# Kernel tuning notes

Measured on AMD Instinct MI355X. Metric: run time of the kernel, lower is better.

## Reference

```python
import jax, jax.numpy as jnp
import numpy as np
import math

N = 100000      # nodes per type
E = 1000000     # edges per edge type
C = 64          # hid_dim_conv (= in_channels)
H = 4           # heads
D = C // H      # head dim
L = 4           # num_conv_layers
T = 3           # node types: op, port, const
REL = [(0, 0), (0, 1), (1, 0), (1, 2), (2, 0)]  # (src_type, dst_type) per edge type
R = len(REL)
POOL = 8
PDIM = 32       # pooling_dim = max(C//2, out_channels)


def _gelu(x):
    return jax.nn.gelu(x, approximate=False)  # torch F.gelu default (erf)


def _seg_softmax(a, seg, n):
    m = jax.ops.segment_max(a, seg, num_segments=n)
    m = jnp.where(jnp.isfinite(m), m, 0.0)
    e = jnp.exp(a - m[seg])
    s = jax.ops.segment_sum(e, seg, num_segments=n)
    return e / (s[seg] + 1e-16)


def _layernorm(x, w, b):
    mu = x.mean(-1, keepdims=True)
    var = ((x - mu) ** 2).mean(-1, keepdims=True)
    return (x - mu) / jnp.sqrt(var + 1e-5) * w + b


def _forward(floats, ints):
    (x0, x1, x2, Wk, bk, Wq, bq, Wv, bv, Wa, ba, skip, ln_w, ln_b,
     a_rel, m_rel, p_rel, Wfc, bfc, Wsc, W1, b1, W2, b2, W3, b3, W4, b4) = floats
    eis = ints
    xs = [x0, x1, x2]
    inv_sqrt_d = 1.0 / math.sqrt(D)
    for l in range(L):
        k = [(xs[t] @ Wk[l, t] + bk[l, t]).reshape(N, H, D) for t in range(T)]
        q = [(xs[t] @ Wq[l, t] + bq[l, t]).reshape(N, H, D) for t in range(T)]
        v = [(xs[t] @ Wv[l, t] + bv[l, t]).reshape(N, H, D) for t in range(T)]
        out = [jnp.zeros((N, H, D), xs[0].dtype) for _ in range(T)]
        for r, (s, d) in enumerate(REL):
            ke = jnp.einsum('nhd,hde->nhe', k[s], a_rel[l, r])  # per-relation key transform
            ve = jnp.einsum('nhd,hde->nhe', v[s], m_rel[l, r])  # per-relation message transform
            row, col = eis[r][0], eis[r][1]
            al = (q[d][col] * ke[row]).sum(-1) * p_rel[l, r] * inv_sqrt_d  # [E,H]
            al = _seg_softmax(al, col, N)
            out[d] = out[d] + jax.ops.segment_sum(ve[row] * al[:, :, None], col, num_segments=N)
        nxs = []
        for t in range(T):
            o = _gelu(out[t].reshape(N, H * D)) @ Wa[l, t] + ba[l, t]
            a = jax.nn.sigmoid(skip[l, t])
            o = a * o + (1.0 - a) * xs[t]
            o = _layernorm(o, ln_w[l, t], ln_b[l, t])
            nxs.append(_gelu(o))
        xs = nxs
    # per-type node_fc, then SAG-style global top-k pooling
    zs = [_gelu(xs[t] @ Wfc[t] + bfc[t]) for t in range(T)]
    z = jnp.concatenate(zs, 0)                              # [T*N, PDIM]
    sc = jnp.concatenate([zs[t] @ Wsc[t] for t in range(T)], 0)  # [T*N]
    ts, ti = jax.lax.top_k(sc, POOL)
    pooled = z[ti] * jnp.tanh(ts)[:, None]                  # [POOL, PDIM]
    h = pooled.reshape(1, POOL * PDIM)
    h = _gelu(h @ W1 + b1)
    h = _gelu(h @ W2 + b2)
    h = _gelu(h @ W3 + b3)
    return jnp.nan_to_num(h @ W4 + b4)


def setup_inputs() -> dict:
    key = jax.random.key(0)
    ks = jax.random.split(key, 24)
    f = jnp.float32
    d = {}
    d['x_op'] = jax.random.normal(ks[0], (N, C), f)
    d['x_port'] = jax.random.normal(ks[1], (N, C), f)
    d['x_const'] = jax.random.normal(ks[2], (N, C), f)
    for i in range(R):
        d[f'ei_{i}'] = jax.random.randint(ks[3 + i], (2, E), 0, N, dtype=jnp.int32)
    s_c = 1.0 / math.sqrt(C)
    s_d = 1.0 / math.sqrt(D)
    d['Wk'] = jax.random.normal(ks[8], (L, T, C, C), f) * s_c
    d['bk'] = jnp.zeros((L, T, C), f)
    d['Wq'] = jax.random.normal(ks[9], (L, T, C, C), f) * s_c
    d['bq'] = jnp.zeros((L, T, C), f)
    d['Wv'] = jax.random.normal(ks[10], (L, T, C, C), f) * s_c
    d['bv'] = jnp.zeros((L, T, C), f)
    d['Wa'] = jax.random.normal(ks[11], (L, T, C, C), f) * s_c
    d['ba'] = jnp.zeros((L, T, C), f)
    d['skip'] = jnp.ones((L, T), f)
    d['ln_w'] = jnp.full((L, T, C), math.sqrt(2.0 / C), f)
    d['ln_b'] = jax.random.normal(ks[12], (L, T, C), f) * 0.01
    d['a_rel'] = jax.random.normal(ks[13], (L, R, H, D, D), f) * s_d
    d['m_rel'] = jax.random.normal(ks[14], (L, R, H, D, D), f) * s_d
    d['p_rel'] = jnp.ones((L, R, H), f)
    d['Wfc'] = jax.random.normal(ks[15], (T, C, PDIM), f) * s_c
    d['bfc'] = jnp.zeros((T, PDIM), f)
    d['Wsc'] = jax.random.normal(ks[16], (T, PDIM), f) * (1.0 / math.sqrt(PDIM))
    d['W1'] = jax.random.normal(ks[17], (POOL * PDIM, 128), f) * (1.0 / math.sqrt(POOL * PDIM))
    d['b1'] = jnp.zeros((128,), f)
    d['W2'] = jax.random.normal(ks[18], (128, 64), f) * (1.0 / math.sqrt(128))
    d['b2'] = jnp.zeros((64,), f)
    d['W3'] = jax.random.normal(ks[19], (64, 32), f) * (1.0 / math.sqrt(64))
    d['b3'] = jnp.zeros((32,), f)
    d['W4'] = jax.random.normal(ks[20], (32, 1), f) * (1.0 / math.sqrt(32))
    d['b4'] = jnp.zeros((1,), f)
    return d


def reference(x_op, x_port, x_const, ei_0, ei_1, ei_2, ei_3, ei_4,
              Wk, bk, Wq, bq, Wv, bv, Wa, ba, skip, ln_w, ln_b,
              a_rel, m_rel, p_rel, Wfc, bfc, Wsc,
              W1, b1, W2, b2, W3, b3, W4, b4):
    floats = (x_op, x_port, x_const, Wk, bk, Wq, bq, Wv, bv, Wa, ba, skip, ln_w, ln_b,
              a_rel, m_rel, p_rel, Wfc, bfc, Wsc, W1, b1, W2, b2, W3, b3, W4, b4)
    ints = (ei_0, ei_1, ei_2, ei_3, ei_4)
    return _forward(floats, ints)
```

## Files before the change

kernel.cpp:

```cpp
#include <hip/hip_runtime.h>
#include <math.h>
#include <float.h>

#define NN 100000
#define EE 1000000
#define CC 64
#define HH 4
#define DD 16
#define LL 4
#define TT 3
#define RR 5
#define NB 196
#define PR 64

__device__ __constant__ int g_dst[RR]   = {0, 1, 0, 2, 0};
__device__ __constant__ int g_first[RR] = {1, 1, 0, 1, 0};

__device__ __forceinline__ float geluf(float x) {
    return 0.5f * x * (1.0f + erff(x * 0.7071067811865476f));
}

__global__ void zero_out_kernel(float* out) {
    if (threadIdx.x == 0 && blockIdx.x == 0) out[0] = 0.f;
}

__device__ __forceinline__ const int* sel_edge(int r, const int* p0, const int* p1,
                                               const int* p2, const int* p3, const int* p4) {
    return (r == 0) ? p0 : (r == 1) ? p1 : (r == 2) ? p2 : (r == 3) ? p3 : p4;
}

__global__ __launch_bounds__(256) void fuse_q(
    const float* __restrict__ Wq, const float* __restrict__ bq,
    const float* __restrict__ a_rel,
    float* __restrict__ WQE, float* __restrict__ BQE)
{
    int lr = blockIdx.x;
    int l = lr / RR, r = lr % RR;
    int d = g_dst[r];
    const float* W  = Wq + (size_t)(l * TT + d) * CC * CC;
    const float* bb = bq + (size_t)(l * TT + d) * CC;
    const float* A  = a_rel + (size_t)lr * HH * DD * DD;
    float* Wo = WQE + (size_t)lr * CC * CC;
    float* bo = BQE + (size_t)lr * CC;

    for (int i = threadIdx.x; i < CC * CC; i += 256) {
        int c = i >> 6, j = i & 63, h = j >> 4, dout = j & 15;
        float acc = 0.f;
        #pragma unroll
        for (int e0 = 0; e0 < DD; ++e0)
            acc += W[c * CC + h * DD + e0] * A[(h * DD + dout) * DD + e0];
        Wo[i] = acc;
    }
    if (threadIdx.x < CC) {
        int j = threadIdx.x, h = j >> 4, dout = j & 15;
        float acc = 0.f;
        #pragma unroll
        for (int e0 = 0; e0 < DD; ++e0)
            acc += bb[h * DD + e0] * A[(h * DD + dout) * DD + e0];
        bo[j] = acc;
    }
}

__global__ __launch_bounds__(256) void bucket_hist(
    const int* __restrict__ p0, const int* __restrict__ p1, const int* __restrict__ p2,
    const int* __restrict__ p3, const int* __restrict__ p4, int* __restrict__ bcnt)
{
    int r = blockIdx.y;
    const int* col = sel_edge(r, p0, p1, p2, p3, p4) + EE;
    __shared__ int lh[256];
    int tid = threadIdx.x;
    lh[tid] = 0;
    __syncthreads();
    int base = blockIdx.x * 4096;
    for (int i = tid; i < 4096; i += 256) {
        int g = base + i;
        if (g < EE) atomicAdd(&lh[col[g] >> 9], 1);
    }
    __syncthreads();
    if (tid < NB && lh[tid]) atomicAdd(&bcnt[r * NB + tid], lh[tid]);
}

__global__ __launch_bounds__(256) void bucket_scan(
    const int* __restrict__ bcnt, int* __restrict__ bbase, int* __restrict__ gcur,
    int* __restrict__ indptr)
{
    int r = blockIdx.x;
    __shared__ int ls[256];
    int tid = threadIdx.x;
    ls[tid] = (tid < NB) ? bcnt[r * NB + tid] : 0;
    __syncthreads();
    for (int o = 1; o < 256; o <<= 1) {
        int v = (tid >= o) ? ls[tid - o] : 0;
        __syncthreads();
        ls[tid] += v;
        __syncthreads();
    }
    int ex = (tid == 0) ? 0 : ls[tid - 1];
    if (tid < NB) {
        bbase[r * (NB + 1) + tid] = ex;
        gcur[r * NB + tid] = ex;
    }
    if (tid == NB) bbase[r * (NB + 1) + NB] = ls[NB - 1];
    if (tid == 0) indptr[(size_t)r * (NN + 1) + NN] = EE;
}

__global__ __launch_bounds__(256) void bucket_partition(
    const int* __restrict__ p0, const int* __restrict__ p1, const int* __restrict__ p2,
    const int* __restrict__ p3, const int* __restrict__ p4,
    int* __restrict__ gcur, unsigned* __restrict__ pairs)
{
    int r = blockIdx.y;
    const int* ebase = sel_edge(r, p0, p1, p2, p3, p4);
    const int* colp = ebase + EE;
    __shared__ int2 stag[4096];
    __shared__ int lh[256], lofs[256], lcur[256], gpos[256];
    int tid = threadIdx.x;
    lh[tid] = 0;
    __syncthreads();
    int base = blockIdx.x * 4096;
    for (int i = tid; i < 4096; i += 256) {
        int g = base + i;
        if (g < EE) atomicAdd(&lh[colp[g] >> 9], 1);
    }
    __syncthreads();
    lofs[tid] = lh[tid];
    __syncthreads();
    for (int o = 1; o < 256; o <<= 1) {
        int v = (tid >= o) ? lofs[tid - o] : 0;
        __syncthreads();
        lofs[tid] += v;
        __syncthreads();
    }
    int ex = (tid == 0) ? 0 : lofs[tid - 1];
    __syncthreads();
    lofs[tid] = ex;
    lcur[tid] = ex;
    gpos[tid] = (lh[tid] > 0) ? atomicAdd(&gcur[r * NB + tid], lh[tid]) : 0;
    __syncthreads();
    for (int i = tid; i < 4096; i += 256) {
        int g = base + i;
        if (g < EE) {
            int c = colp[g];
            int b = c >> 9;
            int s = atomicAdd(&lcur[b], 1);
            stag[s] = make_int2(ebase[g], c);
        }
    }
    __syncthreads();
    int total = EE - base; if (total > 4096) total = 4096;
    for (int s = tid; s < total; s += 256) {
        int2 pr = stag[s];
        int b = pr.y >> 9;
        unsigned packed = ((unsigned)(pr.y & 511) << 17) | (unsigned)pr.x;
        pairs[(size_t)r * EE + gpos[b] + (s - lofs[b])] = packed;
    }
}

__global__ __launch_bounds__(256) void bucket_finalize(
    const unsigned* __restrict__ pairs, const int* __restrict__ bbase,
    int* __restrict__ indptr, int* __restrict__ rowsrt)
{
    int r = blockIdx.y, b = blockIdx.x;
    int beg = bbase[r * (NB + 1) + b], end = bbase[r * (NB + 1) + b + 1];
    int d0 = b << 9;
    int nd = NN - d0; if (nd > 512) nd = 512;
    __shared__ int cnt[512];
    __shared__ int exc[512];
    __shared__ int ls[256];
    int tid = threadIdx.x;
    cnt[tid] = 0; cnt[tid + 256] = 0;
    __syncthreads();
    const unsigned* pp = pairs + (size_t)r * EE;
    for (int e = beg + tid; e < end; e += 256)
        atomicAdd(&cnt[pp[e] >> 17], 1);
    __syncthreads();
    int a0 = cnt[2 * tid], a1 = cnt[2 * tid + 1];
    ls[tid] = a0 + a1;
    __syncthreads();
    for (int o = 1; o < 256; o <<= 1) {
        int v = (tid >= o) ? ls[tid - o] : 0;
        __syncthreads();
        ls[tid] += v;
        __syncthreads();
    }
    int ex2 = (tid == 0) ? 0 : ls[tid - 1];
    exc[2 * tid] = ex2;
    exc[2 * tid + 1] = ex2 + a0;
    __syncthreads();
    for (int i = tid; i < nd; i += 256)
        indptr[(size_t)r * (NN + 1) + d0 + i] = beg + exc[i];
    cnt[2 * tid] = exc[2 * tid];
    cnt[2 * tid + 1] = exc[2 * tid + 1];
    __syncthreads();
    for (int e = beg + tid; e < end; e += 256) {
        unsigned pr = pp[e];
        int p = atomicAdd(&cnt[pr >> 17], 1);
        rowsrt[(size_t)r * EE + beg + p] = (int)(pr & 0x1FFFFu);
    }
}

__global__ __launch_bounds__(256) void projKV_kernel(
    const float* __restrict__ X,
    const float* __restrict__ WK, const float* __restrict__ BK,
    const float* __restrict__ WV, const float* __restrict__ BV,
    float* __restrict__ KV, int nrows)
{
    __shared__ float Xs[PR][CC + 1];
    __shared__ float WKs[CC][CC];
    __shared__ float WVs[CC][CC];
    __shared__ float bks[CC], bvs[CC];
    int tid = threadIdx.x;
    int row0 = blockIdx.x * PR;
    for (int i = tid; i < CC * CC; i += 256) {
        WKs[i >> 6][i & 63] = WK[i];
        WVs[i >> 6][i & 63] = WV[i];
    }
    if (tid < CC) { bks[tid] = BK[tid]; bvs[tid] = BV[tid]; }
    for (int i = tid; i < PR * CC; i += 256) {
        int r = i >> 6, c = i & 63;
        int gr = row0 + r;
        Xs[r][c] = (gr < nrows) ? X[(size_t)gr * CC + c] : 0.f;
    }
    __syncthreads();
    int tx = tid & 15, ty = tid >> 4;
    float aK[4][4], aV[4][4];
    #pragma unroll
    for (int i = 0; i < 4; ++i)
        #pragma unroll
        for (int j = 0; j < 4; ++j) { aK[i][j] = 0.f; aV[i][j] = 0.f; }
    for (int k = 0; k < CC; ++k) {
        float xv[4], wk4[4], wv4[4];
        #pragma unroll
        for (int i = 0; i < 4; ++i) xv[i] = Xs[ty + 16 * i][k];
        #pragma unroll
        for (int j = 0; j < 4; ++j) { wk4[j] = WKs[k][tx + 16 * j]; wv4[j] = WVs[k][tx + 16 * j]; }
        #pragma unroll
        for (int i = 0; i < 4; ++i)
            #pragma unroll
            for (int j = 0; j < 4; ++j) {
                aK[i][j] += xv[i] * wk4[j];
                aV[i][j] += xv[i] * wv4[j];
            }
    }
    #pragma unroll
    for (int i = 0; i < 4; ++i) {
        int r = row0 + ty + 16 * i;
        if (r < nrows) {
            #pragma unroll
            for (int j = 0; j < 4; ++j) {
                int c = tx + 16 * j;
                KV[(size_t)r * 128 + c]      = aK[i][j] + bks[c];
                KV[(size_t)r * 128 + 64 + c] = aV[i][j] + bvs[c];
            }
        }
    }
}

__global__ __launch_bounds__(256) void edge_kernel(
    const int* __restrict__ indptr_all, const int* __restrict__ rows_all,
    const float* __restrict__ x0, const float* __restrict__ x1, const float* __restrict__ x2,
    const float* __restrict__ WQE_l, const float* __restrict__ BQE_l,
    const float* __restrict__ kv, const float* __restrict__ Mrel_l,
    const float* __restrict__ prel_l,
    float* __restrict__ outb, int r0)
{
    int ri = blockIdx.y;
    int r = r0 + ri;
    int d = g_dst[r];
    const float* xd = (d == 0) ? x0 : (d == 1) ? x1 : x2;
    const int* indptr = indptr_all + (size_t)r * (NN + 1);
    const int* rows = rows_all + (size_t)r * EE;
    const float* Wq = WQE_l + (size_t)ri * CC * CC;
    const float* bqp = BQE_l + (size_t)ri * CC;
    const float* Mrel = Mrel_l + (size_t)ri * HH * DD * DD;
    const float* prel = prel_l + (size_t)ri * HH;
    float* outp = outb + (size_t)d * NN * CC;
    int accum = 1 - g_first[r];

    __shared__ float4 Wq4s[CC][16];
    __shared__ float  xs[16][CC + 4];
    __shared__ float4 bq4s[16];
    int tid = threadIdx.x;
    const float4* Wq4 = (const float4*)Wq;
    for (int i = tid; i < CC * 16; i += 256)
        Wq4s[i >> 4][i & 15] = Wq4[i];
    if (tid < 16) bq4s[tid] = ((const float4*)bqp)[tid];
    {
        float4 xv4 = ((const float4*)xd)[(size_t)blockIdx.x * 256 + tid];
        ((float4*)&xs[tid >> 4][0])[tid & 15] = xv4;
    }
    __syncthreads();

    int g = tid >> 4;
    int gl = tid & 15;
    int node = blockIdx.x * 16 + g;
    int h = gl >> 2;
    float ps = prel[h] * (0.25f * 1.4426950408889634f);

    float4 q4 = bq4s[gl];
    #pragma unroll 8
    for (int k = 0; k < CC; ++k) {
        float xk = xs[g][k];
        float4 w = Wq4s[k][gl];
        q4.x += xk * w.x; q4.y += xk * w.y; q4.z += xk * w.z; q4.w += xk * w.w;
    }

    int beg = indptr[node], end = indptr[node + 1];
    float m = -INFINITY, ss = 0.f;
    float4 o4 = make_float4(0.f, 0.f, 0.f, 0.f);
    const float4* kv4 = (const float4*)kv;
    for (int e = beg; e < end; ++e) {
        int rr = rows[e];
        const float4* kp = kv4 + (size_t)rr * 32;
        float4 k4 = kp[gl];
        float4 v4 = kp[16 + gl];
        float p = q4.x * k4.x + q4.y * k4.y + q4.z * k4.z + q4.w * k4.w;
        p += __shfl_xor(p, 1, 4);
        p += __shfl_xor(p, 2, 4);
        float al = p * ps;
        float nm = fmaxf(m, al);
        float sc = exp2f(m - nm);
        float ei = exp2f(al - nm);
        ss = ss * sc + ei;
        o4.x = o4.x * sc + ei * v4.x;
        o4.y = o4.y * sc + ei * v4.y;
        o4.z = o4.z * sc + ei * v4.z;
        o4.w = o4.w * sc + ei * v4.w;
        m = nm;
    }
    float inv = 1.f / (ss + 1e-16f);
    float4 res = make_float4(o4.x * inv, o4.y * inv, o4.z * inv, o4.w * inv);

    const float4* Ms4 = (const float4*)Mrel;
    float4 out4 = make_float4(0.f, 0.f, 0.f, 0.f);
    int e4 = gl & 3;
    #pragma unroll
    for (int sl = 0; sl < 4; ++sl) {
        int src = (gl & 12) + sl;
        float a0 = __shfl(res.x, src, 16);
        float a1 = __shfl(res.y, src, 16);
        float a2 = __shfl(res.z, src, 16);
        float a3 = __shfl(res.w, src, 16);
        float4 m0 = Ms4[(h * DD + sl * 4 + 0) * 4 + e4];
        float4 m1 = Ms4[(h * DD + sl * 4 + 1) * 4 + e4];
        float4 m2 = Ms4[(h * DD + sl * 4 + 2) * 4 + e4];
        float4 m3 = Ms4[(h * DD + sl * 4 + 3) * 4 + e4];
        out4.x += a0 * m0.x + a1 * m1.x + a2 * m2.x + a3 * m3.x;
        out4.y += a0 * m0.y + a1 * m1.y + a2 * m2.y + a3 * m3.y;
        out4.z += a0 * m0.z + a1 * m1.z + a2 * m2.z + a3 * m3.z;
        out4.w += a0 * m0.w + a1 * m1.w + a2 * m2.w + a3 * m3.w;
    }

    float4* op = (float4*)outp + (size_t)node * 16;
    if (accum) {
        float4 old = op[gl];
        out4.x += old.x; out4.y += old.y; out4.z += old.z; out4.w += old.w;
    }
    op[gl] = out4;
}

__global__ __launch_bounds__(256) void post3_kernel(
    const float* __restrict__ x0, const float* __restrict__ x1, const float* __restrict__ x2,
    const float* __restrict__ outc, float* __restrict__ xout,
    const float* __restrict__ Wa_l, const float* __restrict__ ba_l,
    const float* __restrict__ skp_l,
    const float* __restrict__ lnw_l, const float* __restrict__ lnb_l)
{
    int t = blockIdx.y;
    const float* xin = (t == 0) ? x0 : (t == 1) ? x1 : x2;
    const float* Wa = Wa_l + (size_t)t * CC * CC;
    const float* ba = ba_l + (size_t)t * CC;
    const float* lnw = lnw_l + (size_t)t * CC;
    const float* lnb = lnb_l + (size_t)t * CC;
    const float* oc = outc + (size_t)t * NN * CC;
    float* xo = xout + (size_t)t * NN * CC;

    __shared__ float Gs[PR][CC + 1];
    __shared__ float Was[CC][CC];
    __shared__ float bas[CC], lnws[CC], lnbs[CC];
    int tid = threadIdx.x;
    int row0 = blockIdx.x * PR;
    for (int i = tid; i < CC * CC; i += 256) Was[i >> 6][i & 63] = Wa[i];
    if (tid < CC) { bas[tid] = ba[tid]; lnws[tid] = lnw[tid]; lnbs[tid] = lnb[tid]; }
    for (int i = tid; i < PR * CC; i += 256) {
        int r = i >> 6, c = i & 63;
        int gr = row0 + r;
        Gs[r][c] = (gr < NN) ? geluf(oc[(size_t)gr * CC + c]) : 0.f;
    }
    __syncthreads();
    int tx = tid & 15, ty = tid >> 4;
    float acc[4][4];
    #pragma unroll
    for (int i = 0; i < 4; ++i)
        #pragma unroll
        for (int j = 0; j < 4; ++j) acc[i][j] = 0.f;
    for (int k = 0; k < CC; ++k) {
        float gv[4], w4[4];
        #pragma unroll
        for (int i = 0; i < 4; ++i) gv[i] = Gs[ty + 16 * i][k];
        #pragma unroll
        for (int j = 0; j < 4; ++j) w4[j] = Was[k][tx + 16 * j];
        #pragma unroll
        for (int i = 0; i < 4; ++i)
            #pragma unroll
            for (int j = 0; j < 4; ++j) acc[i][j] += gv[i] * w4[j];
    }
    float a = 1.f / (1.f + expf(-skp_l[t]));
    #pragma unroll
    for (int i = 0; i < 4; ++i) {
        int r = row0 + ty + 16 * i;
        if (r >= NN) continue;
        float vals[4];
        float s1 = 0.f;
        #pragma unroll
        for (int j = 0; j < 4; ++j) {
            int c = tx + 16 * j;
            float o = a * (acc[i][j] + bas[c]) + (1.f - a) * xin[(size_t)r * CC + c];
            vals[j] = o;
            s1 += o;
        }
        s1 += __shfl_xor(s1, 1, 16);
        s1 += __shfl_xor(s1, 2, 16);
        s1 += __shfl_xor(s1, 4, 16);
        s1 += __shfl_xor(s1, 8, 16);
        float mean = s1 * (1.f / 64.f);
        float s2 = 0.f;
        #pragma unroll
        for (int j = 0; j < 4; ++j) {
            float dc = vals[j] - mean;
            s2 += dc * dc;
        }
        s2 += __shfl_xor(s2, 1, 16);
        s2 += __shfl_xor(s2, 2, 16);
        s2 += __shfl_xor(s2, 4, 16);
        s2 += __shfl_xor(s2, 8, 16);
        float inv = 1.f / sqrtf(s2 * (1.f / 64.f) + 1e-5f);
        #pragma unroll
        for (int j = 0; j < 4; ++j) {
            int c = tx + 16 * j;
            float y = (vals[j] - mean) * inv * lnws[c] + lnbs[c];
            xo[(size_t)r * CC + c] = geluf(y);
        }
    }
}

__global__ __launch_bounds__(256) void scores_kernel(const float* __restrict__ X,
                                                     const float* __restrict__ Wfc, const float* __restrict__ bfc,
                                                     const float* __restrict__ Wsc, float* __restrict__ sc)
{
    int t = blockIdx.y;
    __shared__ float Xs[PR][CC + 1];
    __shared__ float Wfs[CC][33];
    __shared__ float bfs[32], wscs[32];
    int tid = threadIdx.x;
    int row0 = blockIdx.x * PR;
    const float* Xt = X + (size_t)t * NN * CC;
    for (int i = tid; i < CC * 32; i += 256) Wfs[i >> 5][i & 31] = Wfc[(size_t)t * CC * 32 + i];
    if (tid < 32) { bfs[tid] = bfc[t * 32 + tid]; wscs[tid] = Wsc[t * 32 + tid]; }
    for (int i = tid; i < PR * CC; i += 256) {
        int r = i >> 6, c = i & 63;
        int gr = row0 + r;
        Xs[r][c] = (gr < NN) ? Xt[(size_t)gr * CC + c] : 0.f;
    }
    __syncthreads();
    int tx = tid & 15, ty = tid >> 4;
    float acc[4][2];
    #pragma unroll
    for (int i = 0; i < 4; ++i) { acc[i][0] = 0.f; acc[i][1] = 0.f; }
    for (int k = 0; k < CC; ++k) {
        float w0 = Wfs[k][tx], w1 = Wfs[k][tx + 16];
        #pragma unroll
        for (int i = 0; i < 4; ++i) {
            float xv = Xs[ty + 16 * i][k];
            acc[i][0] += xv * w0;
            acc[i][1] += xv * w1;
        }
    }
    #pragma unroll
    for (int i = 0; i < 4; ++i) {
        float p = geluf(acc[i][0] + bfs[tx]) * wscs[tx]
                + geluf(acc[i][1] + bfs[tx + 16]) * wscs[tx + 16];
        p += __shfl_xor(p, 1, 16);
        p += __shfl_xor(p, 2, 16);
        p += __shfl_xor(p, 4, 16);
        p += __shfl_xor(p, 8, 16);
        int r = row0 + ty + 16 * i;
        if (tx == 0 && r < NN) sc[(size_t)t * NN + r] = p;
    }
}

#define CHUNK 1250
__global__ __launch_bounds__(256) void topk1(const float* __restrict__ sc, float* __restrict__ candv,
                                             int* __restrict__ candi, int total)
{
    __shared__ float v[CHUNK];
    __shared__ float rv[256];
    __shared__ int ri[256];
    int tid = threadIdx.x;
    int base = blockIdx.x * CHUNK;
    for (int i = tid; i < CHUNK; i += 256) {
        int g = base + i;
        v[i] = (g < total) ? sc[g] : -INFINITY;
    }
    __syncthreads();
    for (int it = 0; it < 8; ++it) {
        float bv = v[tid]; int bi = tid;
        for (int i = tid + 256; i < CHUNK; i += 256) {
            float x = v[i];
            if (x > bv) { bv = x; bi = i; }
        }
        rv[tid] = bv; ri[tid] = bi;
        __syncthreads();
        for (int s2 = 128; s2 > 0; s2 >>= 1) {
            if (tid < s2) {
                float ov = rv[tid + s2]; int oi = ri[tid + s2];
                if (ov > rv[tid] || (ov == rv[tid] && oi < ri[tid])) { rv[tid] = ov; ri[tid] = oi; }
            }
            __syncthreads();
        }
        if (tid == 0) {
            candv[blockIdx.x * 8 + it] = rv[0];
            candi[blockIdx.x * 8 + it] = base + ri[0];
            v[ri[0]] = -INFINITY;
        }
        __syncthreads();
    }
}

#define NCAND 1920
__global__ __launch_bounds__(256) void topk2(const float* __restrict__ candv, const int* __restrict__ candi,
                                             float* __restrict__ topv, int* __restrict__ topi)
{
    __shared__ float v[NCAND];
    __shared__ int gi[NCAND];
    __shared__ float rv[256];
    __shared__ int ri[256];
    int tid = threadIdx.x;
    for (int i = tid; i < NCAND; i += 256) { v[i] = candv[i]; gi[i] = candi[i]; }
    __syncthreads();
    for (int it = 0; it < 8; ++it) {
        float bv = v[tid]; int bs = tid;
        for (int i = tid + 256; i < NCAND; i += 256) {
            float x = v[i];
            if (x > bv || (x == bv && gi[i] < gi[bs])) { bv = x; bs = i; }
        }
        rv[tid] = bv; ri[tid] = bs;
        __syncthreads();
        for (int s2 = 128; s2 > 0; s2 >>= 1) {
            if (tid < s2) {
                float ov = rv[tid + s2]; int os = ri[tid + s2];
                if (ov > rv[tid] || (ov == rv[tid] && gi[os] < gi[ri[tid]])) { rv[tid] = ov; ri[tid] = os; }
            }
            __syncthreads();
        }
        if (tid == 0) {
            topv[it] = rv[0];
            topi[it] = gi[ri[0]];
            v[ri[0]] = -INFINITY;
        }
        __syncthreads();
    }
}

__global__ __launch_bounds__(256) void mlp_kernel(const float* __restrict__ X,
    const float* __restrict__ Wfc, const float* __restrict__ bfc,
    const float* __restrict__ topv, const int* __restrict__ topi,
    const float* __restrict__ W1, const float* __restrict__ b1,
    const float* __restrict__ W2, const float* __restrict__ b2,
    const float* __restrict__ W3, const float* __restrict__ b3,
    const float* __restrict__ W4, const float* __restrict__ b4,
    float* __restrict__ out)
{
    __shared__ float h0[256], h1[128], h2[64], h3[32];
    int tid = threadIdx.x;
    int wv = tid >> 6, lane = tid & 63;
    int j = lane & 31, half = lane >> 5;
    for (int w = wv; w < 8; w += 4) {
        int gidx = topi[w];
        float ts = topv[w];
        const float* xr = X + (size_t)gidx * 64;
        int t = gidx / NN;
        const float* Wf = Wfc + (size_t)t * CC * 32;
        float acc = 0.f;
        #pragma unroll
        for (int k2 = 0; k2 < 32; ++k2) {
            int k = half * 32 + k2;
            acc += xr[k] * Wf[k * 32 + j];
        }
        acc += __shfl_xor(acc, 32, 64);
        float z = geluf(acc + bfc[t * 32 + j]);
        if (half == 0) h0[w * 32 + j] = z * tanhf(ts);
    }
    __syncthreads();
    if (tid < 128) {
        float a = b1[tid];
        for (int k = 0; k < 256; ++k) a += h0[k] * W1[k * 128 + tid];
        h1[tid] = geluf(a);
    }
    __syncthreads();
    if (tid < 64) {
        float a = b2[tid];
        for (int k = 0; k < 128; ++k) a += h1[k] * W2[k * 64 + tid];
        h2[tid] = geluf(a);
    }
    __syncthreads();
    if (tid < 32) {
        float a = b3[tid];
        for (int k = 0; k < 64; ++k) a += h2[k] * W3[k * 32 + tid];
        h3[tid] = geluf(a);
    }
    __syncthreads();
    if (tid == 0) {
        float a = b4[0];
        for (int k = 0; k < 32; ++k) a += h3[k] * W4[k];
        if (isnan(a)) a = 0.f;
        else if (isinf(a)) a = (a > 0.f) ? FLT_MAX : -FLT_MAX;
        out[0] = a;
    }
}

extern "C" void kernel_launch(void* const* d_in, const int* in_sizes, int n_in,
                              void* d_out, int out_size, void* d_ws, size_t ws_size,
                              hipStream_t stream)
{
    (void)in_sizes; (void)n_in; (void)out_size;
    static const int h_r0[TT]   = {0, 2, 4};
    static const int h_nrel[TT] = {2, 2, 1};

    const float* xin0[TT] = {(const float*)d_in[0], (const float*)d_in[1], (const float*)d_in[2]};
    const int* ei[RR];
    for (int r = 0; r < RR; ++r) ei[r] = (const int*)d_in[3 + r];
    const float* Wk   = (const float*)d_in[8];
    const float* bk   = (const float*)d_in[9];
    const float* Wq   = (const float*)d_in[10];
    const float* bq   = (const float*)d_in[11];
    const float* Wv   = (const float*)d_in[12];
    const float* bv   = (const float*)d_in[13];
    const float* Wa   = (const float*)d_in[14];
    const float* ba   = (const float*)d_in[15];
    const float* skp  = (const float*)d_in[16];
    const float* lnw  = (const float*)d_in[17];
    const float* lnb  = (const float*)d_in[18];
    const float* a_rel = (const float*)d_in[19];
    const float* m_rel = (const float*)d_in[20];
    const float* p_rel = (const float*)d_in[21];
    const float* Wfc  = (const float*)d_in[22];
    const float* bfc  = (const float*)d_in[23];
    const float* Wsc  = (const float*)d_in[24];
    const float* W1 = (const float*)d_in[25]; const float* b1 = (const float*)d_in[26];
    const float* W2 = (const float*)d_in[27]; const float* b2 = (const float*)d_in[28];
    const float* W3 = (const float*)d_in[29]; const float* b3 = (const float*)d_in[30];
    const float* W4 = (const float*)d_in[31]; const float* b4 = (const float*)d_in[32];

    char* ws = (char*)d_ws;
    size_t off = 0;
    auto alloc = [&](size_t bytes) -> char* {
        char* p = ws + off;
        off = (off + bytes + 255) & ~(size_t)255;
        return p;
    };
    float* Xb   = (float*)alloc((size_t)TT * NN * CC * 4);
    float* OUTb = (float*)alloc((size_t)TT * NN * CC * 4);
    float* KVb  = (float*)alloc((size_t)NN * 128 * 4);
    float* WQE  = (float*)alloc((size_t)LL * RR * CC * CC * 4);
    float* BQE  = (float*)alloc((size_t)LL * RR * CC * 4);
    int* indptr = (int*)alloc((size_t)RR * (NN + 1) * 4);
    int* rowsrt = (int*)alloc((size_t)RR * EE * 4);
    int* bcnt   = (int*)alloc((size_t)RR * NB * 4);
    int* bbase  = (int*)alloc((size_t)RR * (NB + 1) * 4);
    int* gcur   = (int*)alloc((size_t)RR * NB * 4);
    float* scb  = (float*)alloc((size_t)TT * NN * 4);
    float* candv = (float*)alloc(240 * 8 * 4);
    int* candi   = (int*)alloc(240 * 8 * 4);
    float* topv  = (float*)alloc(64);
    int* topi    = (int*)alloc(64);
    unsigned* pairs = (unsigned*)OUTb;

    if (off > ws_size) {
        zero_out_kernel<<<1, 64, 0, stream>>>((float*)d_out);
        return;
    }

    fuse_q<<<LL * RR, 256, 0, stream>>>(Wq, bq, a_rel, WQE, BQE);

    const int chunkGrid = (EE + 4095) / 4096;
    hipMemsetAsync(bcnt, 0, (size_t)RR * NB * 4, stream);
    bucket_hist<<<dim3(chunkGrid, RR), 256, 0, stream>>>(ei[0], ei[1], ei[2], ei[3], ei[4], bcnt);
    bucket_scan<<<RR, 256, 0, stream>>>(bcnt, bbase, gcur, indptr);
    bucket_partition<<<dim3(chunkGrid, RR), 256, 0, stream>>>(ei[0], ei[1], ei[2], ei[3], ei[4],
                                                              gcur, pairs);
    bucket_finalize<<<dim3(NB, RR), 256, 0, stream>>>(pairs, bbase, indptr, rowsrt);

    const int gproj = (NN + PR - 1) / PR;
    const int gedge = NN / 16;
    const float* xcur[TT] = {xin0[0], xin0[1], xin0[2]};

    for (int l = 0; l < LL; ++l) {
        for (int s = 0; s < TT; ++s) {
            projKV_kernel<<<gproj, 256, 0, stream>>>(xcur[s],
                Wk + (size_t)(l * TT + s) * CC * CC, bk + (size_t)(l * TT + s) * CC,
                Wv + (size_t)(l * TT + s) * CC * CC, bv + (size_t)(l * TT + s) * CC,
                KVb, NN);
            int r0 = h_r0[s];
            int lr0 = l * RR + r0;
            edge_kernel<<<dim3(gedge, h_nrel[s]), 256, 0, stream>>>(
                indptr, rowsrt, xcur[0], xcur[1], xcur[2],
                WQE + (size_t)lr0 * CC * CC, BQE + (size_t)lr0 * CC,
                KVb, m_rel + (size_t)lr0 * HH * DD * DD, p_rel + (size_t)lr0 * HH,
                OUTb, r0);
        }
        post3_kernel<<<dim3(gproj, TT), 256, 0, stream>>>(xcur[0], xcur[1], xcur[2],
            OUTb, Xb,
            Wa + (size_t)l * TT * CC * CC, ba + (size_t)l * TT * CC,
            skp + l * TT,
            lnw + (size_t)l * TT * CC, lnb + (size_t)l * TT * CC);
        for (int t = 0; t < TT; ++t) xcur[t] = Xb + (size_t)t * NN * CC;
    }

    scores_kernel<<<dim3(gproj, TT), 256, 0, stream>>>(Xb, Wfc, bfc, Wsc, scb);
    topk1<<<240, 256, 0, stream>>>(scb, candv, candi, TT * NN);
    topk2<<<1, 256, 0, stream>>>(candv, candi, topv, topi);
    mlp_kernel<<<1, 256, 0, stream>>>(Xb, Wfc, bfc, topv, topi,
                                      W1, b1, W2, b2, W3, b3, W4, b4, (float*)d_out);
}
```

Baseline: 3.009 ms.

## Sort destination nodes by in-degree to balance edge kernel work

Adds a one-time counting sort of destination nodes by in-degree (capped at 255) for each relation, and the edge kernel now processes nodes in that order. Each 16-node block then holds nodes of similar degree, which cuts wave divergence and tail imbalance in the per-node edge loop. The cost is three small preprocessing kernels and the loss of contiguous node access: x rows are gathered via the order array and outputs are scattered.

```diff
diff --git a/kernel.cpp b/kernel.cpp
--- a/kernel.cpp
+++ b/kernel.cpp
@@ -199,6 +199,48 @@
     }
 }
 
+__global__ void deg_hist(const int* __restrict__ indptr, int* __restrict__ dbin)
+{
+    int r = blockIdx.y;
+    int i = blockIdx.x * 256 + threadIdx.x;
+    if (i < NN) {
+        const int* ip = indptr + (size_t)r * (NN + 1);
+        int deg = ip[i + 1] - ip[i];
+        if (deg > 255) deg = 255;
+        atomicAdd(&dbin[r * 256 + deg], 1);
+    }
+}
+
+__global__ __launch_bounds__(256) void deg_scan(int* __restrict__ dbin)
+{
+    int r = blockIdx.x;
+    __shared__ int ls[256];
+    int tid = threadIdx.x;
+    ls[tid] = dbin[r * 256 + tid];
+    __syncthreads();
+    for (int o = 1; o < 256; o <<= 1) {
+        int v = (tid >= o) ? ls[tid - o] : 0;
+        __syncthreads();
+        ls[tid] += v;
+        __syncthreads();
+    }
+    dbin[r * 256 + tid] = (tid == 0) ? 0 : ls[tid - 1];
+}
+
+__global__ void deg_scatter(const int* __restrict__ indptr, int* __restrict__ dbin,
+                            int* __restrict__ order)
+{
+    int r = blockIdx.y;
+    int i = blockIdx.x * 256 + threadIdx.x;
+    if (i < NN) {
+        const int* ip = indptr + (size_t)r * (NN + 1);
+        int deg = ip[i + 1] - ip[i];
+        if (deg > 255) deg = 255;
+        int pos = atomicAdd(&dbin[r * 256 + deg], 1);
+        order[(size_t)r * NN + pos] = i;
+    }
+}
+
 __global__ __launch_bounds__(256) void projKV_kernel(
     const float* __restrict__ X,
     const float* __restrict__ WK, const float* __restrict__ BK,
@@ -258,6 +300,7 @@
 
 __global__ __launch_bounds__(256) void edge_kernel(
     const int* __restrict__ indptr_all, const int* __restrict__ rows_all,
+    const int* __restrict__ order_all,
     const float* __restrict__ x0, const float* __restrict__ x1, const float* __restrict__ x2,
     const float* __restrict__ WQE_l, const float* __restrict__ BQE_l,
     const float* __restrict__ kv, const float* __restrict__ Mrel_l,
@@ -270,6 +313,7 @@
     const float* xd = (d == 0) ? x0 : (d == 1) ? x1 : x2;
     const int* indptr = indptr_all + (size_t)r * (NN + 1);
     const int* rows = rows_all + (size_t)r * EE;
+    const int* order = order_all + (size_t)r * NN;
     const float* Wq = WQE_l + (size_t)ri * CC * CC;
     const float* bqp = BQE_l + (size_t)ri * CC;
     const float* Mrel = Mrel_l + (size_t)ri * HH * DD * DD;
@@ -285,15 +329,16 @@
     for (int i = tid; i < CC * 16; i += 256)
         Wq4s[i >> 4][i & 15] = Wq4[i];
     if (tid < 16) bq4s[tid] = ((const float4*)bqp)[tid];
-    {
-        float4 xv4 = ((const float4*)xd)[(size_t)blockIdx.x * 256 + tid];
-        ((float4*)&xs[tid >> 4][0])[tid & 15] = xv4;
-    }
-    __syncthreads();
 
     int g = tid >> 4;
     int gl = tid & 15;
-    int node = blockIdx.x * 16 + g;
+    int node = order[blockIdx.x * 16 + g];
+    {
+        float4 xv4 = ((const float4*)xd)[(size_t)node * 16 + gl];
+        ((float4*)&xs[g][0])[gl] = xv4;
+    }
+    __syncthreads();
+
     int h = gl >> 2;
     float ps = prel[h] * (0.25f * 1.4426950408889634f);
 
@@ -666,9 +711,11 @@
     float* BQE  = (float*)alloc((size_t)LL * RR * CC * 4);
     int* indptr = (int*)alloc((size_t)RR * (NN + 1) * 4);
     int* rowsrt = (int*)alloc((size_t)RR * EE * 4);
+    int* order  = (int*)alloc((size_t)RR * NN * 4);
     int* bcnt   = (int*)alloc((size_t)RR * NB * 4);
     int* bbase  = (int*)alloc((size_t)RR * (NB + 1) * 4);
     int* gcur   = (int*)alloc((size_t)RR * NB * 4);
+    int* dbin   = (int*)alloc((size_t)RR * 256 * 4);
     float* scb  = (float*)alloc((size_t)TT * NN * 4);
     float* candv = (float*)alloc(240 * 8 * 4);
     int* candi   = (int*)alloc(240 * 8 * 4);
@@ -684,12 +731,18 @@
     fuse_q<<<LL * RR, 256, 0, stream>>>(Wq, bq, a_rel, WQE, BQE);
 
     const int chunkGrid = (EE + 4095) / 4096;
+    const int nGrid = (NN + 255) / 256;
     hipMemsetAsync(bcnt, 0, (size_t)RR * NB * 4, stream);
     bucket_hist<<<dim3(chunkGrid, RR), 256, 0, stream>>>(ei[0], ei[1], ei[2], ei[3], ei[4], bcnt);
     bucket_scan<<<RR, 256, 0, stream>>>(bcnt, bbase, gcur, indptr);
     bucket_partition<<<dim3(chunkGrid, RR), 256, 0, stream>>>(ei[0], ei[1], ei[2], ei[3], ei[4],
                                                               gcur, pairs);
     bucket_finalize<<<dim3(NB, RR), 256, 0, stream>>>(pairs, bbase, indptr, rowsrt);
+
+    hipMemsetAsync(dbin, 0, (size_t)RR * 256 * 4, stream);
+    deg_hist<<<dim3(nGrid, RR), 256, 0, stream>>>(indptr, dbin);
+    deg_scan<<<RR, 256, 0, stream>>>(dbin);
+    deg_scatter<<<dim3(nGrid, RR), 256, 0, stream>>>(indptr, dbin, order);
 
     const int gproj = (NN + PR - 1) / PR;
     const int gedge = NN / 16;
@@ -704,7 +757,7 @@
             int r0 = h_r0[s];
             int lr0 = l * RR + r0;
             edge_kernel<<<dim3(gedge, h_nrel[s]), 256, 0, stream>>>(
-                indptr, rowsrt, xcur[0], xcur[1], xcur[2],
+                indptr, rowsrt, order, xcur[0], xcur[1], xcur[2],
                 WQE + (size_t)lr0 * CC * CC, BQE + (size_t)lr0 * CC,
                 KVb, m_rel + (size_t)lr0 * HH * DD * DD, p_rel + (size_t)lr0 * HH,
                 OUTb, r0);
```

After: 4.078 ms. 1.36x slower.
